# Kernel tuning notes

Hardware: AMD Instinct MI355X
Metric: run time of the kernel (lower is better)

The kernel has to match this reference:

```python
import jax, jax.numpy as jnp
import numpy as np

N, D, I, E, TOPK = 2048, 1024, 2048, 8, 2


def setup_inputs() -> dict:
    key = jax.random.key(0)
    ks = jax.random.split(key, 5)
    s = 0.02  # init scale for weights
    return {
        "x": jax.random.normal(ks[0], (N, D), dtype=jnp.float32),
        "w_router": jax.random.normal(ks[1], (D, E), dtype=jnp.float32) * s,
        "w_gate": jax.random.normal(ks[2], (E, D, I), dtype=jnp.float32) * s,
        "w_up": jax.random.normal(ks[3], (E, D, I), dtype=jnp.float32) * s,
        "w_down": jax.random.normal(ks[4], (E, I, D), dtype=jnp.float32) * s,
        "top_k": TOPK,
    }


def reference(x, w_router, w_gate, w_up, w_down, top_k):
    # Router: top-k logits -> softmax over the selected k only
    logits = x @ w_router                                  # [N, E]
    topk_v, topk_i = jax.lax.top_k(logits, top_k)          # [N, k]
    probs = jax.nn.softmax(topk_v, axis=-1)                # [N, k]
    n_experts = w_gate.shape[0]
    # Per-token per-expert combine weight (0 for unselected experts)
    gates = jnp.sum(jax.nn.one_hot(topk_i, n_experts, dtype=probs.dtype)
                    * probs[..., None], axis=1)            # [N, E]
    # SwiGLU experts, batched over the expert axis
    g = jnp.einsum('nd,edi->eni', x, w_gate)               # [E, N, I]
    u = jnp.einsum('nd,edi->eni', x, w_up)                 # [E, N, I]
    h = jax.nn.silu(g) * u                                 # [E, N, I]
    y = jnp.einsum('eni,eid->end', h, w_down)              # [E, N, D]
    # Weighted combine across experts
    out = jnp.einsum('end,ne->nd', y, gates)               # [N, D]
    return out
```

## Files before the change

kernel.cpp:

```cpp
#include <hip/hip_runtime.h>
#include <hip/hip_bf16.h>
#include <stdint.h>


#define N_TOK 2048
#define DIM   1024
#define IDIM  2048
#define NEXP  8

typedef short s16x8 __attribute__((ext_vector_type(8)));
typedef float f32x4 __attribute__((ext_vector_type(4)));

__device__ __align__(256) __hip_bfloat16 g_xb [(size_t)N_TOK*DIM];
__device__ __align__(256) __hip_bfloat16 g_wgT[(size_t)NEXP*IDIM*DIM];
__device__ __align__(256) __hip_bfloat16 g_wuT[(size_t)NEXP*IDIM*DIM];
__device__ __align__(256) __hip_bfloat16 g_wdT[(size_t)NEXP*DIM*IDIM];
__device__ __align__(256) __hip_bfloat16 g_h  [(size_t)N_TOK*2*IDIM];
__device__ __align__(256) float          g_y  [(size_t)2*N_TOK*2*DIM];
__device__ int   g_topi[N_TOK*2];
__device__ float g_topp[N_TOK*2];
__device__ int   g_rows[N_TOK*2];
__device__ int   g_slot[N_TOK*2];
__device__ float g_probs[N_TOK*2];
__device__ int   g_meta[32];

__device__ __forceinline__ void load_lds16(const void* g, void* l){
  __builtin_amdgcn_global_load_lds(
      (const __attribute__((address_space(1))) unsigned int*)g,
      (__attribute__((address_space(3))) unsigned int*)l, 16, 0, 0);
}

__global__ void k_cast_x(const float* __restrict__ x){
  if (blockIdx.x == 0 && threadIdx.x < 32) g_meta[threadIdx.x] = 0;
  int i = blockIdx.x*256 + threadIdx.x;
  float4 v = ((const float4*)x)[i];
  union { ushort4 u; __hip_bfloat16 b[4]; } o;
  o.b[0] = __float2bfloat16(v.x); o.b[1] = __float2bfloat16(v.y);
  o.b[2] = __float2bfloat16(v.z); o.b[3] = __float2bfloat16(v.w);
  ((ushort4*)g_xb)[i] = o.u;
}

__global__ void k_transpose(const float* __restrict__ wg, const float* __restrict__ wu,
                            const float* __restrict__ wd){
  __shared__ float tile[64][65];
  const int which = blockIdx.z;
  const int e     = blockIdx.y;
  const int R = (which == 2) ? IDIM : DIM;
  const int C = (which == 2) ? DIM  : IDIM;
  const float* src = ((which == 0) ? wg : (which == 1) ? wu : wd) + (size_t)e*DIM*IDIM;
  __hip_bfloat16* dst = ((which == 0) ? g_wgT : (which == 1) ? g_wuT : g_wdT) + (size_t)e*DIM*IDIM;
  const int ntr = R >> 6;
  const int tr = blockIdx.x % ntr, tc = blockIdx.x / ntr;
  const int r0 = tr*64, c0 = tc*64;
  const int t = threadIdx.x;
  #pragma unroll
  for (int it = 0; it < 4; ++it){
    int s = t + it*256; int ri = s >> 4, c4 = (s & 15)*4;
    float4 v = *(const float4*)(src + (size_t)(r0+ri)*C + c0 + c4);
    tile[ri][c4+0] = v.x; tile[ri][c4+1] = v.y; tile[ri][c4+2] = v.z; tile[ri][c4+3] = v.w;
  }
  __syncthreads();
  #pragma unroll
  for (int it = 0; it < 4; ++it){
    int s = t + it*256; int ci = s >> 4, r4 = (s & 15)*4;
    union { ushort4 u; __hip_bfloat16 b[4]; } o;
    #pragma unroll
    for (int j = 0; j < 4; ++j) o.b[j] = __float2bfloat16(tile[r4+j][ci]);
    *(ushort4*)((unsigned short*)dst + (size_t)(c0+ci)*R + r0 + r4) = o.u;
  }
}

__global__ void k_router(const float* __restrict__ x, const float* __restrict__ wr){
  const int w = threadIdx.x >> 6, lane = threadIdx.x & 63;
  const int n = blockIdx.x*4 + w;
  float acc[8] = {0,0,0,0,0,0,0,0};
  const float* xrow = x + (size_t)n*DIM;
  #pragma unroll
  for (int i = 0; i < 16; ++i){
    int d = lane + i*64;
    float xv = xrow[d];
    const float4* wp = (const float4*)(wr + (size_t)d*8);
    float4 w0 = wp[0], w1 = wp[1];
    acc[0] += xv*w0.x; acc[1] += xv*w0.y; acc[2] += xv*w0.z; acc[3] += xv*w0.w;
    acc[4] += xv*w1.x; acc[5] += xv*w1.y; acc[6] += xv*w1.z; acc[7] += xv*w1.w;
  }
  #pragma unroll
  for (int e = 0; e < 8; ++e)
    #pragma unroll
    for (int off = 32; off; off >>= 1) acc[e] += __shfl_xor(acc[e], off);
  if (lane == 0){
    int i0 = -1, i1 = -1; float m0 = -1e30f, m1 = -1e30f;
    #pragma unroll
    for (int e = 0; e < 8; ++e){
      float v = acc[e];
      if (v > m0){ m1 = m0; i1 = i0; m0 = v; i0 = e; }
      else if (v > m1){ m1 = v; i1 = e; }
    }
    float ex = expf(m1 - m0);
    float p0 = 1.f/(1.f+ex), p1 = ex/(1.f+ex);
    g_topi[n*2]   = i0; g_topi[n*2+1] = i1;
    g_topp[n*2]   = p0; g_topp[n*2+1] = p1;
    atomicAdd(&g_meta[i0], 1); atomicAdd(&g_meta[i1], 1);
  }
}

__global__ void k_scan_scatter(){
  if (threadIdx.x == 0){
    int a = 0;
    for (int e = 0; e < 8; ++e){ g_meta[16+e] = a; a += g_meta[e]; }
    g_meta[24] = a;
  }
  __syncthreads();
  for (int it = 0; it < N_TOK/256; ++it){
    const int n = it*256 + threadIdx.x;
    #pragma unroll
    for (int s = 0; s < 2; ++s){
      int e = g_topi[n*2+s]; float p = g_topp[n*2+s];
      int pos = atomicAdd(&g_meta[8+e], 1);
      int slot = g_meta[16+e] + pos;
      g_rows [slot] = n;
      g_probs[slot] = p;
      g_slot [n*2+s] = slot;
    }
  }
}

__global__ __launch_bounds__(256, 4) void k_mlp1(){
  const int e = blockIdx.z;
  const int flat  = blockIdx.x + 16*blockIdx.y;
  const int flat2 = (flat & 7)*64 + (flat >> 3);
  const int tm = flat2 & 15, ti = flat2 >> 4;
  const int cnt = g_meta[e];
  if (tm*128 >= cnt) return;
  const int off = g_meta[16+e];
  __shared__ __align__(16) __hip_bfloat16 lA [2][128*32];
  __shared__ __align__(16) __hip_bfloat16 lBg[2][64*32];
  __shared__ __align__(16) __hip_bfloat16 lBu[2][64*32];
  const int t = threadIdx.x, w = t >> 6, lane = t & 63;
  const int r  = t >> 2, kq = t & 3;
  const int swb = ((kq ^ (r & 3) ^ ((r >> 2) & 3)) << 4);
  const int tok0 = g_rows[off + min(tm*128 + r,      cnt-1)];
  const int tok1 = g_rows[off + min(tm*128 + r + 64, cnt-1)];
  const char* sA0 = (const char*)(g_xb + (size_t)tok0*DIM) + swb;
  const char* sA1 = (const char*)(g_xb + (size_t)tok1*DIM) + swb;
  const size_t wB = ((size_t)e*IDIM + (size_t)ti*64)*DIM;
  const char* sG0 = (const char*)(g_wgT + wB + (size_t)r*DIM) + swb;
  const char* sU0 = (const char*)(g_wuT + wB + (size_t)r*DIM) + swb;
  const int dA = w*1024;
  auto stage = [&](int b, int ks){
    const int kb = ks*64;
    load_lds16(sA0+kb, (char*)lA [b] + dA);
    load_lds16(sA1+kb, (char*)lA [b] + dA + 4096);
    load_lds16(sG0+kb, (char*)lBg[b] + dA);
    load_lds16(sU0+kb, (char*)lBu[b] + dA);
  };
  f32x4 accg[4][2] = {}, accu[4][2] = {};
  const int wr = w >> 1, wc = w & 1;
  const int l15 = lane & 15;
  const int swr = (((lane >> 4) ^ (lane & 3) ^ ((lane >> 2) & 3)) << 4);
  const int aOff = (wr*64 + l15)*64 + swr;
  const int bOff = (wc*32 + l15)*64 + swr;
  stage(0, 0);
  __syncthreads();
  for (int ks = 0; ks < DIM/32; ++ks){
    const int cur = ks & 1;
    if (ks + 1 < DIM/32) stage(cur ^ 1, ks + 1);
    s16x8 af[4], bg[2], bu[2];
    #pragma unroll
    for (int m = 0; m < 4; ++m)
      af[m] = *(const s16x8*)((const char*)lA [cur] + aOff + m*1024);
    #pragma unroll
    for (int n = 0; n < 2; ++n){
      bg[n] = *(const s16x8*)((const char*)lBg[cur] + bOff + n*1024);
      bu[n] = *(const s16x8*)((const char*)lBu[cur] + bOff + n*1024);
    }
    #pragma unroll
    for (int m = 0; m < 4; ++m)
      #pragma unroll
      for (int n = 0; n < 2; ++n){
        accg[m][n] = __builtin_amdgcn_mfma_f32_16x16x32_bf16(af[m], bg[n], accg[m][n], 0, 0, 0);
        accu[m][n] = __builtin_amdgcn_mfma_f32_16x16x32_bf16(af[m], bu[n], accu[m][n], 0, 0, 0);
      }
    __syncthreads();
  }
  const int rbase = wr*64 + ((lane >> 4) << 2);
  const int cbase = ti*64 + wc*32 + l15;
  #pragma unroll
  for (int m = 0; m < 4; ++m){
    #pragma unroll
    for (int j = 0; j < 4; ++j){
      const int lr = rbase + m*16 + j;
      const int gi = tm*128 + lr;
      if (gi < cnt){
        __hip_bfloat16* hp = g_h + (size_t)(off + gi)*IDIM + cbase;
        #pragma unroll
        for (int n = 0; n < 2; ++n){
          float gv = accg[m][n][j], uv = accu[m][n][j];
          float hv = gv / (1.f + __expf(-gv)) * uv;
          hp[n*16] = __float2bfloat16(hv);
        }
      }
    }
  }
}

__global__ __launch_bounds__(256, 4) void k_mlp2(){
  const int e = blockIdx.z;
  const int flat  = blockIdx.x + 16*blockIdx.y;
  const int flat2 = (flat & 7)*64 + (flat >> 3);
  const int tm = flat2 & 15, bdks = flat2 >> 4;
  const int bd = bdks & 15, kh = bdks >> 4;
  const int cnt = g_meta[e];
  if (tm*128 >= cnt) return;
  const int off = g_meta[16+e];
  __shared__ __align__(16) __hip_bfloat16 lA[2][128*32];
  __shared__ __align__(16) __hip_bfloat16 lB[2][64*32];
  const int t = threadIdx.x, w = t >> 6, lane = t & 63;
  const int r  = t >> 2, kq = t & 3;
  const int swb = ((kq ^ (r & 3) ^ ((r >> 2) & 3)) << 4);
  const int h0 = off + min(tm*128 + r,      cnt-1);
  const int h1 = off + min(tm*128 + r + 64, cnt-1);
  const size_t khOff = (size_t)kh*1024*2;
  const char* sA0 = (const char*)(g_h + (size_t)h0*IDIM) + khOff + swb;
  const char* sA1 = (const char*)(g_h + (size_t)h1*IDIM) + khOff + swb;
  const size_t wB = ((size_t)e*DIM + (size_t)bd*64 + r)*IDIM;
  const char* sB0 = (const char*)(g_wdT + wB) + khOff + swb;
  const int dA = w*1024;
  auto stage = [&](int b, int ks){
    const int kb = ks*64;
    load_lds16(sA0+kb, (char*)lA[b] + dA);
    load_lds16(sA1+kb, (char*)lA[b] + dA + 4096);
    load_lds16(sB0+kb, (char*)lB[b] + dA);
  };
  f32x4 acc[4][2] = {};
  const int wr = w >> 1, wc = w & 1;
  const int l15 = lane & 15;
  const int swr = (((lane >> 4) ^ (lane & 3) ^ ((lane >> 2) & 3)) << 4);
  const int aOff = (wr*64 + l15)*64 + swr;
  const int bOff = (wc*32 + l15)*64 + swr;
  stage(0, 0);
  __syncthreads();
  for (int ks = 0; ks < 32; ++ks){
    const int cur = ks & 1;
    if (ks + 1 < 32) stage(cur ^ 1, ks + 1);
    s16x8 af[4], bw[2];
    #pragma unroll
    for (int m = 0; m < 4; ++m)
      af[m] = *(const s16x8*)((const char*)lA[cur] + aOff + m*1024);
    #pragma unroll
    for (int n = 0; n < 2; ++n)
      bw[n] = *(const s16x8*)((const char*)lB[cur] + bOff + n*1024);
    #pragma unroll
    for (int m = 0; m < 4; ++m)
      #pragma unroll
      for (int n = 0; n < 2; ++n)
        acc[m][n] = __builtin_amdgcn_mfma_f32_16x16x32_bf16(af[m], bw[n], acc[m][n], 0, 0, 0);
    __syncthreads();
  }
  const int rbase = wr*64 + ((lane >> 4) << 2);
  const int cb = bd*64 + wc*32 + l15;
  #pragma unroll
  for (int m = 0; m < 4; ++m){
    #pragma unroll
    for (int j = 0; j < 4; ++j){
      const int lr = rbase + m*16 + j;
      const int gi = tm*128 + lr;
      if (gi < cnt){
        float* yp = g_y + ((size_t)kh*(N_TOK*2) + (off + gi))*DIM + cb;
        #pragma unroll
        for (int n = 0; n < 2; ++n)
          yp[n*16] = acc[m][n][j];
      }
    }
  }
}

__global__ void k_combine(float* __restrict__ out){
  const int n = blockIdx.x, t = threadIdx.x;
  const int s0 = g_slot[n*2], s1 = g_slot[n*2+1];
  const float p0 = g_probs[s0], p1 = g_probs[s1];
  const float4* y0 = (const float4*)g_y;
  const float4* y1 = (const float4*)(g_y + (size_t)(N_TOK*2)*DIM);
  float4 a0 = y0[(size_t)s0*(DIM/4) + t], a1 = y1[(size_t)s0*(DIM/4) + t];
  float4 b0 = y0[(size_t)s1*(DIM/4) + t], b1 = y1[(size_t)s1*(DIM/4) + t];
  float4 o;
  o.x = p0*(a0.x+a1.x) + p1*(b0.x+b1.x);
  o.y = p0*(a0.y+a1.y) + p1*(b0.y+b1.y);
  o.z = p0*(a0.z+a1.z) + p1*(b0.z+b1.z);
  o.w = p0*(a0.w+a1.w) + p1*(b0.w+b1.w);
  ((float4*)(out + (size_t)n*DIM))[t] = o;
}

extern "C" void kernel_launch(void* const* d_in, const int* in_sizes, int n_in,
                              void* d_out, int out_size, void* d_ws, size_t ws_size,
                              hipStream_t stream){
  (void)in_sizes; (void)n_in; (void)d_ws; (void)ws_size; (void)out_size;
  const float* x  = (const float*)d_in[0];
  const float* wr = (const float*)d_in[1];
  const float* wg = (const float*)d_in[2];
  const float* wu = (const float*)d_in[3];
  const float* wd = (const float*)d_in[4];
  float* out = (float*)d_out;

  k_cast_x      <<<2048, 256, 0, stream>>>(x);
  k_router      <<<N_TOK/4, 256, 0, stream>>>(x, wr);
  k_scan_scatter<<<1, 256, 0, stream>>>();
  k_transpose   <<<dim3(512, NEXP, 3), 256, 0, stream>>>(wg, wu, wd);
  k_mlp1        <<<dim3(16, 32, NEXP), 256, 0, stream>>>();
  k_mlp2        <<<dim3(16, 32, NEXP), 256, 0, stream>>>();
  k_combine     <<<N_TOK, 256, 0, stream>>>(out);
}
```

Baseline: 414.3 us.

## Parallelize expert scatter per-expert with ballot scan and widen transpose tiles

Replaces the single-block atomic scan/scatter with one block per expert. Each block counts tokens by comparison and assigns slots with a ballot prefix scan, which also removes the atomic counters and the g_meta reset. The weight transpose now converts to bf16 before staging in LDS, uses 128x64 tiles, and writes 16-byte stores instead of 8-byte ones. This cuts LDS traffic and launches half as many blocks. The aim is to shorten the serial scatter and the bandwidth-heavy transpose, at the cost of each scatter block rereading all top-k indices.

```diff
diff --git a/kernel.cpp b/kernel.cpp
--- a/kernel.cpp
+++ b/kernel.cpp
@@ -31,7 +31,6 @@
 }
 
 __global__ void k_cast_x(const float* __restrict__ x){
-  if (blockIdx.x == 0 && threadIdx.x < 32) g_meta[threadIdx.x] = 0;
   int i = blockIdx.x*256 + threadIdx.x;
   float4 v = ((const float4*)x)[i];
   union { ushort4 u; __hip_bfloat16 b[4]; } o;
@@ -40,33 +39,52 @@
   ((ushort4*)g_xb)[i] = o.u;
 }
 
-__global__ void k_transpose(const float* __restrict__ wg, const float* __restrict__ wu,
-                            const float* __restrict__ wd){
-  __shared__ float tile[64][65];
+__global__ __launch_bounds__(256) void k_transpose(const float* __restrict__ wg,
+                                                   const float* __restrict__ wu,
+                                                   const float* __restrict__ wd){
+  __shared__ __align__(16) __hip_bfloat16 tile[64][132];
   const int which = blockIdx.z;
   const int e     = blockIdx.y;
   const int R = (which == 2) ? IDIM : DIM;
   const int C = (which == 2) ? DIM  : IDIM;
   const float* src = ((which == 0) ? wg : (which == 1) ? wu : wd) + (size_t)e*DIM*IDIM;
   __hip_bfloat16* dst = ((which == 0) ? g_wgT : (which == 1) ? g_wuT : g_wdT) + (size_t)e*DIM*IDIM;
-  const int ntr = R >> 6;
+  const int ntr = R >> 7;
   const int tr = blockIdx.x % ntr, tc = blockIdx.x / ntr;
-  const int r0 = tr*64, c0 = tc*64;
+  const int r0 = tr*128, c0 = tc*64;
   const int t = threadIdx.x;
+  const int c4 = (t & 15)*4;
+  #pragma unroll
+  for (int it = 0; it < 2; ++it){
+    const int r4 = ((t >> 4) + it*16)*4;
+    const float* sp = src + (size_t)(r0 + r4)*C + c0 + c4;
+    float4 v0 = *(const float4*)(sp);
+    float4 v1 = *(const float4*)(sp + C);
+    float4 v2 = *(const float4*)(sp + 2*C);
+    float4 v3 = *(const float4*)(sp + 3*C);
+    union { __hip_bfloat16 b[4]; ushort4 u; } q;
+    q.b[0]=__float2bfloat16(v0.x); q.b[1]=__float2bfloat16(v1.x);
+    q.b[2]=__float2bfloat16(v2.x); q.b[3]=__float2bfloat16(v3.x);
+    *(ushort4*)&tile[c4+0][r4] = q.u;
+    q.b[0]=__float2bfloat16(v0.y); q.b[1]=__float2bfloat16(v1.y);
+    q.b[2]=__float2bfloat16(v2.y); q.b[3]=__float2bfloat16(v3.y);
+    *(ushort4*)&tile[c4+1][r4] = q.u;
+    q.b[0]=__float2bfloat16(v0.z); q.b[1]=__float2bfloat16(v1.z);
+    q.b[2]=__float2bfloat16(v2.z); q.b[3]=__float2bfloat16(v3.z);
+    *(ushort4*)&tile[c4+2][r4] = q.u;
+    q.b[0]=__float2bfloat16(v0.w); q.b[1]=__float2bfloat16(v1.w);
+    q.b[2]=__float2bfloat16(v2.w); q.b[3]=__float2bfloat16(v3.w);
+    *(ushort4*)&tile[c4+3][r4] = q.u;
+  }
+  __syncthreads();
   #pragma unroll
   for (int it = 0; it < 4; ++it){
-    int s = t + it*256; int ri = s >> 4, c4 = (s & 15)*4;
-    float4 v = *(const float4*)(src + (size_t)(r0+ri)*C + c0 + c4);
-    tile[ri][c4+0] = v.x; tile[ri][c4+1] = v.y; tile[ri][c4+2] = v.z; tile[ri][c4+3] = v.w;
-  }
-  __syncthreads();
-  #pragma unroll
-  for (int it = 0; it < 4; ++it){
-    int s = t + it*256; int ci = s >> 4, r4 = (s & 15)*4;
-    union { ushort4 u; __hip_bfloat16 b[4]; } o;
-    #pragma unroll
-    for (int j = 0; j < 4; ++j) o.b[j] = __float2bfloat16(tile[r4+j][ci]);
-    *(ushort4*)((unsigned short*)dst + (size_t)(c0+ci)*R + r0 + r4) = o.u;
+    const int s = t + it*256;
+    const int ci = s >> 4, r8 = (s & 15)*8;
+    ushort4 a = *(const ushort4*)&tile[ci][r8];
+    ushort4 b = *(const ushort4*)&tile[ci][r8+4];
+    union { ushort4 u[2]; uint4 v; } q; q.u[0] = a; q.u[1] = b;
+    *(uint4*)((unsigned short*)dst + (size_t)(c0+ci)*R + r0 + r8) = q.v;
   }
 }
 
@@ -100,28 +118,48 @@
     float p0 = 1.f/(1.f+ex), p1 = ex/(1.f+ex);
     g_topi[n*2]   = i0; g_topi[n*2+1] = i1;
     g_topp[n*2]   = p0; g_topp[n*2+1] = p1;
-    atomicAdd(&g_meta[i0], 1); atomicAdd(&g_meta[i1], 1);
-  }
-}
-
-__global__ void k_scan_scatter(){
-  if (threadIdx.x == 0){
-    int a = 0;
-    for (int e = 0; e < 8; ++e){ g_meta[16+e] = a; a += g_meta[e]; }
-    g_meta[24] = a;
-  }
-  __syncthreads();
-  for (int it = 0; it < N_TOK/256; ++it){
-    const int n = it*256 + threadIdx.x;
-    #pragma unroll
-    for (int s = 0; s < 2; ++s){
-      int e = g_topi[n*2+s]; float p = g_topp[n*2+s];
-      int pos = atomicAdd(&g_meta[8+e], 1);
-      int slot = g_meta[16+e] + pos;
-      g_rows [slot] = n;
-      g_probs[slot] = p;
-      g_slot [n*2+s] = slot;
-    }
+  }
+}
+
+__global__ void k_scatter(){
+  const int e = blockIdx.x;
+  __shared__ int wsum[4];
+  const int t = threadIdx.x, w = t >> 6, lane = t & 63;
+  int clt = 0, ceq = 0;
+  for (int s = t; s < N_TOK*2; s += 256){
+    int v = g_topi[s];
+    clt += (v < e); ceq += (v == e);
+  }
+  int p = clt | (ceq << 16);
+  #pragma unroll
+  for (int o = 32; o; o >>= 1) p += __shfl_xor(p, o);
+  if (lane == 0) wsum[w] = p;
+  __syncthreads();
+  const int tot = wsum[0] + wsum[1] + wsum[2] + wsum[3];
+  const int off = tot & 0xFFFF, cnt = tot >> 16;
+  if (t == 0){ g_meta[e] = cnt; g_meta[16+e] = off; }
+  __syncthreads();
+  int run = off;
+  for (int s0 = 0; s0 < N_TOK*2; s0 += 256){
+    const int s = s0 + t;
+    const bool m = (g_topi[s] == e);
+    unsigned long long mask = __ballot(m);
+    int pre  = __popcll(mask & ((1ULL << lane) - 1ULL));
+    int wcnt = __popcll(mask);
+    if (lane == 0) wsum[w] = wcnt;
+    __syncthreads();
+    int wbase = 0;
+    #pragma unroll
+    for (int i = 0; i < 4; ++i) if (i < w) wbase += wsum[i];
+    const int itot = wsum[0] + wsum[1] + wsum[2] + wsum[3];
+    if (m){
+      int slot = run + wbase + pre;
+      g_rows [slot] = s >> 1;
+      g_probs[slot] = g_topp[s];
+      g_slot [s]    = slot;
+    }
+    run += itot;
+    __syncthreads();
   }
 }
 
@@ -302,11 +340,11 @@
   const float* wd = (const float*)d_in[4];
   float* out = (float*)d_out;
 
-  k_cast_x      <<<2048, 256, 0, stream>>>(x);
-  k_router      <<<N_TOK/4, 256, 0, stream>>>(x, wr);
-  k_scan_scatter<<<1, 256, 0, stream>>>();
-  k_transpose   <<<dim3(512, NEXP, 3), 256, 0, stream>>>(wg, wu, wd);
-  k_mlp1        <<<dim3(16, 32, NEXP), 256, 0, stream>>>();
-  k_mlp2        <<<dim3(16, 32, NEXP), 256, 0, stream>>>();
-  k_combine     <<<N_TOK, 256, 0, stream>>>(out);
-}
+  k_cast_x   <<<2048, 256, 0, stream>>>(x);
+  k_router   <<<N_TOK/4, 256, 0, stream>>>(x, wr);
+  k_scatter  <<<NEXP, 256, 0, stream>>>();
+  k_transpose<<<dim3(256, NEXP, 3), 256, 0, stream>>>(wg, wu, wd);
+  k_mlp1     <<<dim3(16, 32, NEXP), 256, 0, stream>>>();
+  k_mlp2     <<<dim3(16, 32, NEXP), 256, 0, stream>>>();
+  k_combine  <<<N_TOK, 256, 0, stream>>>(out);
+}
```

Measured after the change: 349.8 us. 15.6% less time.
